# Optimization experiments

Hardware: AMD Instinct MI355X
Metric: run time of the kernel (lower is better)

The kernel has to match this reference:

```python
import jax, jax.numpy as jnp
import numpy as np

ORDER = 2  # diffusion steps per support
NUM_LAYERS = 2


def gconv(z, supports, W, b):
    # z: [B,N,C]; supports: [S,N,N]; concat [z, S1 z, S1^2 z, S2 z, S2^2 z] -> dense proj
    feats = [z]
    for si in range(supports.shape[0]):
        s = supports[si]
        zk = z
        for _ in range(ORDER):
            zk = jnp.einsum('mn,bnc->bmc', s, zk)
            feats.append(zk)
    zcat = jnp.concatenate(feats, axis=-1)  # [B,N,C*(1+S*ORDER)]
    return zcat @ W + b


def dcgru_cell(x, h, supports, Wg, bg, Wc, bc):
    H = h.shape[-1]
    zr = jax.nn.sigmoid(gconv(jnp.concatenate([x, h], axis=-1), supports, Wg, bg))
    z, r = zr[..., :H], zr[..., H:]
    hc = jnp.tanh(gconv(jnp.concatenate([x, r * h], axis=-1), supports, Wc, bc))
    return z * h + (1.0 - z) * hc


def setup_inputs() -> dict:
    key = jax.random.key(0)
    ks = jax.random.split(key, 32)
    B, T, N, D_IN, H = 64, 12, 325, 2, 128
    K = 1 + 2 * ORDER  # 5 diffusion matrices
    inp = {}
    inp['source'] = jax.random.normal(ks[0], (B, T, N, D_IN), jnp.float32)
    inp['targets'] = jax.random.normal(ks[1], (B, T, N, D_IN), jnp.float32)
    u = jax.random.uniform(ks[2], (2, N, N), jnp.float32)
    inp['supports'] = u / jnp.sum(u, axis=-1, keepdims=True)  # row-stochastic random walks
    sc = 0.05
    inp['enc_Wg0'] = sc * jax.random.normal(ks[3], ((D_IN + H) * K, 2 * H), jnp.float32)
    inp['enc_bg0'] = jnp.zeros((2 * H,), jnp.float32)
    inp['enc_Wc0'] = sc * jax.random.normal(ks[4], ((D_IN + H) * K, H), jnp.float32)
    inp['enc_bc0'] = jnp.zeros((H,), jnp.float32)
    inp['enc_Wg1'] = sc * jax.random.normal(ks[5], ((H + H) * K, 2 * H), jnp.float32)
    inp['enc_bg1'] = jnp.zeros((2 * H,), jnp.float32)
    inp['enc_Wc1'] = sc * jax.random.normal(ks[6], ((H + H) * K, H), jnp.float32)
    inp['enc_bc1'] = jnp.zeros((H,), jnp.float32)
    inp['dec_Wg0'] = sc * jax.random.normal(ks[7], ((D_IN + H) * K, 2 * H), jnp.float32)
    inp['dec_bg0'] = jnp.zeros((2 * H,), jnp.float32)
    inp['dec_Wc0'] = sc * jax.random.normal(ks[8], ((D_IN + H) * K, H), jnp.float32)
    inp['dec_bc0'] = jnp.zeros((H,), jnp.float32)
    inp['dec_Wg1'] = sc * jax.random.normal(ks[9], ((H + H) * K, 2 * H), jnp.float32)
    inp['dec_bg1'] = jnp.zeros((2 * H,), jnp.float32)
    inp['dec_Wc1'] = sc * jax.random.normal(ks[10], ((H + H) * K, H), jnp.float32)
    inp['dec_bc1'] = jnp.zeros((H,), jnp.float32)
    inp['Wp'] = sc * jax.random.normal(ks[11], (H, D_IN), jnp.float32)
    inp['bp'] = jnp.zeros((D_IN,), jnp.float32)
    return inp


def _forward(source, targets, supports,
             enc_Wg0, enc_bg0, enc_Wc0, enc_bc0, enc_Wg1, enc_bg1, enc_Wc1, enc_bc1,
             dec_Wg0, dec_bg0, dec_Wc0, dec_bc0, dec_Wg1, dec_bg1, dec_Wc1, dec_bc1,
             Wp, bp):
    B, T_in, N, D_in = source.shape
    T_out = targets.shape[1]
    enc_params = [(enc_Wg0, enc_bg0, enc_Wc0, enc_bc0), (enc_Wg1, enc_bg1, enc_Wc1, enc_bc1)]
    dec_params = [(dec_Wg0, dec_bg0, dec_Wc0, dec_bc0), (dec_Wg1, dec_bg1, dec_Wc1, dec_bc1)]

    # ---- encoder: per layer, scan over time ----
    cur = jnp.swapaxes(source, 0, 1)  # [T,B,N,C]
    enc_finals = []
    for (Wg, bg, Wc, bc) in enc_params:
        H = Wc.shape[-1]
        h0 = jnp.zeros((B, N, H), source.dtype)
        def step(h, xt, Wg=Wg, bg=bg, Wc=Wc, bc=bc):
            h2 = dcgru_cell(xt, h, supports, Wg, bg, Wc, bc)
            return h2, h2
        hT, hs = jax.lax.scan(step, h0, cur)
        enc_finals.append(hT)
        cur = hs

    # ---- decoder (teacher_forcing_ratio = 0 for determinism) ----
    out_dim = Wp.shape[-1]
    go = jnp.zeros((B, N, out_dim), source.dtype)  # GO symbol

    def dec_step(carry, _):
        states, cur_in = carry
        new_states = []
        x = cur_in
        for i, (Wg, bg, Wc, bc) in enumerate(dec_params):
            s = dcgru_cell(x, states[i], supports, Wg, bg, Wc, bc)
            x = s
            new_states.append(s)
        out = jnp.einsum('bnh,ho->bno', x, Wp) + bp  # [B,N,out_dim]
        return (tuple(new_states), out), out

    _, outs = jax.lax.scan(dec_step, (tuple(enc_finals), go), None, length=T_out)
    return jnp.swapaxes(outs, 0, 1)  # [B,T_out,N,out_dim]


def reference(source, targets, supports,
              enc_Wg0, enc_bg0, enc_Wc0, enc_bc0, enc_Wg1, enc_bg1, enc_Wc1, enc_bc1,
              dec_Wg0, dec_bg0, dec_Wc0, dec_bc0, dec_Wg1, dec_bg1, dec_Wc1, dec_bc1,
              Wp, bp):
    return _forward(source, targets, supports,
                    enc_Wg0, enc_bg0, enc_Wc0, enc_bc0, enc_Wg1, enc_bg1, enc_Wc1, enc_bc1,
                    dec_Wg0, dec_bg0, dec_Wc0, dec_bc0, dec_Wg1, dec_bg1, dec_Wc1, dec_bc1,
                    Wp, bp)
```

## Files before the change

kernel.cpp:

```cpp
#include <hip/hip_runtime.h>
#include <hip/hip_bf16.h>

#define B_  64
#define T_  12
#define N_  325
#define DIN 2
#define H_  128
#define BN  (B_*N_)
#define DPITCH 384
#define AROWS 384

typedef __hip_bfloat16 bf16;
typedef unsigned short u16;
typedef __attribute__((ext_vector_type(8))) short short8;
typedef __attribute__((ext_vector_type(4))) float f32x4;

__device__ __forceinline__ float b2f(bf16 v){ return __bfloat162float(v); }
__device__ __forceinline__ u16 f2b(float f){
    __hip_bfloat16 h = __float2bfloat16(f);
    return *reinterpret_cast<u16*>(&h);
}
__device__ __forceinline__ float ldf(const void* p, size_t i, int bf){
    return bf ? b2f(((const bf16*)p)[i]) : ((const float*)p)[i];
}

__device__ __forceinline__ void gl_lds16(const u16* g, u16* l){
    __builtin_amdgcn_global_load_lds(
        (const __attribute__((address_space(1))) unsigned int*)g,
        (__attribute__((address_space(3))) unsigned int*)l, 16, 0, 0);
}

struct FillCfg { u16 *F, *Ft; const float *x, *h; long xbs; int C, KC, Cpad, Din, b0, nb; };
struct DiffCfg { u16* F; const u16* Ft; int C, KC, Cpad, coff, ctiles, T, nb; };
struct GemmCfg { const u16* Fb; const u16* Wt; const float* bias; float* zr; float* hb;
                 int KC, KCpad, rows, gy, ct, nb; };
struct RhCfg  { u16 *F, *Ft; const float *zr, *h; int KC, Cpad, Din, b0, total, nb; };

__global__ void sniff(const void* __restrict__ sup, int* __restrict__ flag){
    if (threadIdx.x == 0 && blockIdx.x == 0){
        float sb = 0.f, sf = 0.f;
        for (int n = 0; n < N_; ++n){
            sb += b2f(((const bf16*)sup)[n]);
            sf += ((const float*)sup)[n];
        }
        float db = fabsf(sb - 1.f), df = fabsf(sf - 1.f);
        *flag = (db < df) ? 1 : 0;
    }
}

struct CvtArgs { const void* src[12]; float* dst[12]; int n[12]; };

__global__ void cvt_all(CvtArgs a, const int* __restrict__ flag){
    int ii = blockIdx.y;
    int i  = blockIdx.x*256 + threadIdx.x;
    if (i >= a.n[ii]) return;
    a.dst[ii][i] = ldf(a.src[ii], i, *flag);
}

__global__ void support_prep(const void* __restrict__ sup, const int* __restrict__ flag,
                             float* __restrict__ msq){
    int bf = *flag;
    int s = blockIdx.z;
    int m = blockIdx.y*16 + threadIdx.y;
    int n = blockIdx.x*16 + threadIdx.x;
    __shared__ float As[16][17], Bs[16][17];
    size_t base = (size_t)s*N_*N_;
    float acc = 0.f;
    for (int j0 = 0; j0 < N_; j0 += 16){
        As[threadIdx.y][threadIdx.x] = (m < N_ && j0+threadIdx.x < N_) ? ldf(sup, base + (size_t)m*N_ + j0+threadIdx.x, bf) : 0.f;
        Bs[threadIdx.y][threadIdx.x] = (j0+threadIdx.y < N_ && n < N_) ? ldf(sup, base + (size_t)(j0+threadIdx.y)*N_ + n, bf) : 0.f;
        __syncthreads();
        #pragma unroll
        for (int jj=0; jj<16; ++jj) acc += As[threadIdx.y][jj]*Bs[jj][threadIdx.x];
        __syncthreads();
    }
    if (m < N_ && n < N_){
        msq[(size_t)(2*s  )*N_*N_ + m*N_ + n] = ldf(sup, base + (size_t)m*N_ + n, bf);
        msq[(size_t)(2*s+1)*N_*N_ + m*N_ + n] = acc;
    }
}

__global__ void asq_prep(const float* __restrict__ msq, u16* __restrict__ asq){
    int idx = blockIdx.x*256 + threadIdx.x;
    int total = 4*AROWS*DPITCH;
    if (idx >= total) return;
    int col = idx % DPITCH;
    int rm  = idx / DPITCH;
    int m   = rm % AROWS;
    int k   = rm / AROWS;
    asq[idx] = (m < N_ && col < N_) ? f2b(msq[((size_t)k*N_ + m)*N_ + col]) : 0;
}

__global__ __launch_bounds__(256) void wtrans(const void* __restrict__ W, u16* __restrict__ Wt,
                                              int KC, int Nout, int KCpad,
                                              const int* __restrict__ flag){
    int bf = *flag;
    int k0 = blockIdx.x*64, c0 = blockIdx.y*64;
    int tid = threadIdx.x;
    __shared__ u16 T[64][72];
    #pragma unroll
    for (int it=0; it<2; ++it){
        int lin = it*256 + tid;
        int kl = lin >> 3, seg = lin & 7;
        int gk = k0 + kl, gc = c0 + seg*8;
        u16 tmp[8];
        #pragma unroll
        for (int e=0;e<8;++e) tmp[e] = (gk < KC) ? f2b(ldf(W, (size_t)gk*Nout + gc + e, bf)) : 0;
        *(uint4*)&T[kl][seg*8] = *(const uint4*)tmp;
    }
    __syncthreads();
    #pragma unroll
    for (int it=0; it<2; ++it){
        int lin = it*256 + tid;
        int cl = lin >> 3, seg = lin & 7;
        u16 tmp[8];
        #pragma unroll
        for (int j=0;j<8;++j) tmp[j] = T[seg*8+j][cl];
        *(uint4*)(Wt + (size_t)(c0+cl)*KCpad + k0 + seg*8) = *(const uint4*)tmp;
    }
}

__global__ __launch_bounds__(256) void fill_k(FillCfg ca, FillCfg cb, int na){
    int bi = blockIdx.x;
    FillCfg c = ca;
    if (bi >= na){ c = cb; bi -= na; }
    int gyc  = c.Cpad >> 6;
    int nblk = bi % 6;
    int rest = bi / 6;
    int cblk = rest % gyc;
    int bl   = rest / gyc;
    int bg = c.b0 + bl;
    int n0 = nblk*64, c0 = cblk*64;
    int tid = threadIdx.x;
    __shared__ u16 T[64][72];
    #pragma unroll
    for (int it=0; it<2; ++it){
        int lin = it*256 + tid;
        int nl = lin >> 3, seg = lin & 7;
        int gn = n0 + nl;
        u16 tmp[8];
        #pragma unroll
        for (int e=0;e<8;++e){
            int cc = c0 + seg*8 + e;
            float v = 0.f;
            if (gn < N_ && cc < c.C)
                v = (cc < c.Din) ? c.x[(size_t)bg*c.xbs + (size_t)gn*c.Din + cc]
                                 : c.h[((size_t)bg*N_ + gn)*H_ + (cc - c.Din)];
            tmp[e] = f2b(v);
        }
        *(uint4*)&T[nl][seg*8] = *(const uint4*)tmp;
        if (gn < N_){
            int cbase = c0 + seg*8;
            u16* dst = c.F + ((size_t)bl*N_ + gn)*c.KC + cbase;
            if (cbase + 7 < c.C){
                *(uint4*)dst = *(const uint4*)tmp;
            } else {
                #pragma unroll
                for (int e=0;e<8;++e) if (cbase + e < c.C) dst[e] = tmp[e];
            }
        }
    }
    __syncthreads();
    #pragma unroll
    for (int it=0; it<2; ++it){
        int lin = it*256 + tid;
        int cl = lin >> 3, seg = lin & 7;
        u16 tmp[8];
        #pragma unroll
        for (int j=0;j<8;++j) tmp[j] = T[seg*8+j][cl];
        *(uint4*)(c.Ft + (size_t)bl*c.Cpad*DPITCH + (size_t)(c0+cl)*DPITCH + n0 + seg*8)
            = *(const uint4*)tmp;
    }
}

__global__ void rh_k(RhCfg ca, RhCfg cb, int na){
    int blk = blockIdx.x;
    RhCfg c = ca;
    if (blk >= na){ c = cb; blk -= na; }
    int idx = blk*256 + threadIdx.x;
    if (idx >= c.total) return;
    int j   = idx & 127;
    int bnl = idx >> 7;
    int bl  = bnl / N_;
    int n   = bnl % N_;
    float r  = c.zr[(size_t)bnl*256 + 128 + j];
    float hv = c.h[((size_t)c.b0*N_ + bnl)*128 + j];
    u16 v = f2b(r * hv);
    c.F[(size_t)bnl*c.KC + c.Din + j] = v;
    c.Ft[((size_t)bl*c.Cpad + c.Din + j)*DPITCH + n] = v;
}

__global__ __launch_bounds__(256) void diffuse_k(DiffCfg ca, DiffCfg cb, int na,
                                                 const u16* __restrict__ asq){
    int bi = blockIdx.x;
    DiffCfg c = ca;
    if (bi >= na){ c = cb; bi -= na; }
    int xcd = bi & 7, m8 = bi >> 3;
    int tg = m8 / 12, s = m8 % 12;
    int t = tg*8 + xcd;
    if (t >= c.T) return;
    int bl = t / c.ctiles, cbk = t % c.ctiles;
    int y = s % 3, k = s / 3;

    const u16* A    = asq + (size_t)k*AROWS*DPITCH;
    const u16* Bt_g = c.Ft + ((size_t)bl*c.Cpad + c.coff)*DPITCH;
    u16*       Cm   = c.F + (size_t)bl*N_*c.KC + (size_t)(k+1)*c.C + c.coff;

    int m0 = y * 128;
    int c0 = cbk * 64;
    int tid = threadIdx.x;
    int wv = tid >> 6, lane = tid & 63, l15 = lane & 15, quad = lane >> 4;
    int lr = lane >> 3, ls = lane & 7;

    __shared__ u16 As[128*64];
    __shared__ u16 Bs[64*64];

    f32x4 acc[2][4];
    #pragma unroll
    for (int i2=0;i2<2;++i2)
        #pragma unroll
        for (int j=0;j<4;++j) acc[i2][j] = (f32x4){0.f,0.f,0.f,0.f};

    for (int k0 = 0; k0 < N_; k0 += 64){
        #pragma unroll
        for (int j=0;j<4;++j){
            int row = wv*32 + j*8 + lr;
            int seg = ls ^ lr;
            gl_lds16(A + (size_t)(m0+row)*DPITCH + k0 + seg*8, &As[(wv*32 + j*8)*64]);
        }
        #pragma unroll
        for (int j=0;j<2;++j){
            int row = wv*16 + j*8 + lr;
            int seg = ls ^ lr;
            gl_lds16(Bt_g + (size_t)(c0+row)*DPITCH + k0 + seg*8, &Bs[(wv*16 + j*8)*64]);
        }
        __syncthreads();
        #pragma unroll
        for (int ks = 0; ks < 64; ks += 32){
            int sw = (((ks>>3) + quad) ^ (l15 & 7)) << 3;
            short8 a0 = *(const short8*)&As[(wv*32      + l15)*64 + sw];
            short8 a1 = *(const short8*)&As[(wv*32 + 16 + l15)*64 + sw];
            short8 b0 = *(const short8*)&Bs[(     l15)*64 + sw];
            short8 b1 = *(const short8*)&Bs[(16 + l15)*64 + sw];
            short8 b2 = *(const short8*)&Bs[(32 + l15)*64 + sw];
            short8 b3 = *(const short8*)&Bs[(48 + l15)*64 + sw];
            acc[0][0] = __builtin_amdgcn_mfma_f32_16x16x32_bf16(a0,b0,acc[0][0],0,0,0);
            acc[0][1] = __builtin_amdgcn_mfma_f32_16x16x32_bf16(a0,b1,acc[0][1],0,0,0);
            acc[0][2] = __builtin_amdgcn_mfma_f32_16x16x32_bf16(a0,b2,acc[0][2],0,0,0);
            acc[0][3] = __builtin_amdgcn_mfma_f32_16x16x32_bf16(a0,b3,acc[0][3],0,0,0);
            acc[1][0] = __builtin_amdgcn_mfma_f32_16x16x32_bf16(a1,b0,acc[1][0],0,0,0);
            acc[1][1] = __builtin_amdgcn_mfma_f32_16x16x32_bf16(a1,b1,acc[1][1],0,0,0);
            acc[1][2] = __builtin_amdgcn_mfma_f32_16x16x32_bf16(a1,b2,acc[1][2],0,0,0);
            acc[1][3] = __builtin_amdgcn_mfma_f32_16x16x32_bf16(a1,b3,acc[1][3],0,0,0);
        }
        __syncthreads();
    }
    #pragma unroll
    for (int i2=0;i2<2;++i2){
        #pragma unroll
        for (int j=0;j<4;++j){
            int cc = c0 + j*16 + l15;
            #pragma unroll
            for (int r=0;r<4;++r){
                int m = m0 + wv*32 + i2*16 + quad*4 + r;
                if (m < N_ && c.coff + cc < c.C) Cm[(size_t)m*c.KC + cc] = f2b(acc[i2][j][r]);
            }
        }
    }
}

template<int MODE>
__global__ __launch_bounds__(256) void gemm_k(GemmCfg ca, GemmCfg cb, int na){
    int bi = blockIdx.x;
    GemmCfg c = ca;
    if (bi >= na){ c = cb; bi -= na; }
    int xcd = bi & 7, q = bi >> 3;
    int cbk = q % c.ct;
    int rt  = (q / c.ct)*8 + xcd;
    if (rt >= c.gy) return;
    int r0 = rt * 128;
    int c0 = cbk * 64;
    int tid = threadIdx.x;
    int wv = tid >> 6, lane = tid & 63, l15 = lane & 15, quad = lane >> 4;
    int lr = lane >> 3, ls = lane & 7;

    __shared__ u16 As[128*64];
    __shared__ u16 Bs[64*64];

    f32x4 acc[2][4];
    #pragma unroll
    for (int i2=0;i2<2;++i2)
        #pragma unroll
        for (int j=0;j<4;++j) acc[i2][j] = (f32x4){0.f,0.f,0.f,0.f};

    for (int k0 = 0; k0 < c.KCpad; k0 += 64){
        if (k0 + 64 <= c.KC){
            #pragma unroll
            for (int j=0;j<4;++j){
                int row = wv*32 + j*8 + lr;
                int seg = ls ^ lr;
                gl_lds16(c.Fb + (size_t)(r0+row)*c.KC + k0 + seg*8, &As[(wv*32 + j*8)*64]);
            }
        } else {
            #pragma unroll
            for (int it=0; it<4; ++it){
                int lin = it*256 + tid;
                int row = lin >> 3, sp = lin & 7;
                int seg = sp ^ (row & 7);
                int gr = r0 + row, gk = k0 + seg*8;
                u16 tmp[8];
                #pragma unroll
                for (int e=0;e<8;++e)
                    tmp[e] = (gk+e < c.KC) ? c.Fb[(size_t)gr*c.KC + gk+e] : (u16)0;
                *(uint4*)&As[row*64 + sp*8] = *(const uint4*)tmp;
            }
        }
        #pragma unroll
        for (int j=0;j<2;++j){
            int row = wv*16 + j*8 + lr;
            int seg = ls ^ lr;
            gl_lds16(c.Wt + (size_t)(c0+row)*c.KCpad + k0 + seg*8, &Bs[(wv*16 + j*8)*64]);
        }
        __syncthreads();
        #pragma unroll
        for (int ks = 0; ks < 64; ks += 32){
            int sw = (((ks>>3) + quad) ^ (l15 & 7)) << 3;
            short8 a0 = *(const short8*)&As[(wv*32      + l15)*64 + sw];
            short8 a1 = *(const short8*)&As[(wv*32 + 16 + l15)*64 + sw];
            short8 b0 = *(const short8*)&Bs[(     l15)*64 + sw];
            short8 b1 = *(const short8*)&Bs[(16 + l15)*64 + sw];
            short8 b2 = *(const short8*)&Bs[(32 + l15)*64 + sw];
            short8 b3 = *(const short8*)&Bs[(48 + l15)*64 + sw];
            acc[0][0] = __builtin_amdgcn_mfma_f32_16x16x32_bf16(a0,b0,acc[0][0],0,0,0);
            acc[0][1] = __builtin_amdgcn_mfma_f32_16x16x32_bf16(a0,b1,acc[0][1],0,0,0);
            acc[0][2] = __builtin_amdgcn_mfma_f32_16x16x32_bf16(a0,b2,acc[0][2],0,0,0);
            acc[0][3] = __builtin_amdgcn_mfma_f32_16x16x32_bf16(a0,b3,acc[0][3],0,0,0);
            acc[1][0] = __builtin_amdgcn_mfma_f32_16x16x32_bf16(a1,b0,acc[1][0],0,0,0);
            acc[1][1] = __builtin_amdgcn_mfma_f32_16x16x32_bf16(a1,b1,acc[1][1],0,0,0);
            acc[1][2] = __builtin_amdgcn_mfma_f32_16x16x32_bf16(a1,b2,acc[1][2],0,0,0);
            acc[1][3] = __builtin_amdgcn_mfma_f32_16x16x32_bf16(a1,b3,acc[1][3],0,0,0);
        }
        __syncthreads();
    }
    #pragma unroll
    for (int i2=0;i2<2;++i2){
        #pragma unroll
        for (int j=0;j<4;++j){
            int cc = c0 + j*16 + l15;
            #pragma unroll
            for (int r=0;r<4;++r){
                int gr = r0 + wv*32 + i2*16 + quad*4 + r;
                if (gr >= c.rows) continue;
                float v = acc[i2][j][r] + c.bias[cc];
                if (MODE == 0){
                    v = 1.f/(1.f + __expf(-v));
                    c.zr[(size_t)gr*256 + cc] = v;
                } else {
                    float hc   = tanhf(v);
                    float z    = c.zr[(size_t)gr*256 + cc];
                    float hold = c.hb[(size_t)gr*128 + cc];
                    c.hb[(size_t)gr*128 + cc] = z*hold + (1.f - z)*hc;
                }
            }
        }
    }
}

__global__ __launch_bounds__(256) void proj(const float* __restrict__ h1,
                                            const float* __restrict__ Wp,
                                            const float* __restrict__ bp,
                                            float* __restrict__ xdec,
                                            float* __restrict__ out, int t){
    int row  = blockIdx.x * 4 + (threadIdx.x >> 6);
    int lane = threadIdx.x & 63;
    float v0 = h1[(size_t)row*128 + lane];
    float v1 = h1[(size_t)row*128 + 64 + lane];
    float w00 = Wp[lane*2+0],      w01 = Wp[lane*2+1];
    float w10 = Wp[(64+lane)*2+0], w11 = Wp[(64+lane)*2+1];
    float a0 = v0*w00 + v1*w10;
    float a1 = v0*w01 + v1*w11;
    #pragma unroll
    for (int off=32; off>0; off>>=1){
        a0 += __shfl_down(a0, off);
        a1 += __shfl_down(a1, off);
    }
    if (lane == 0){
        a0 += bp[0];
        a1 += bp[1];
        xdec[(size_t)row*2+0] = a0;
        xdec[(size_t)row*2+1] = a1;
        int b = row / N_, n = row % N_;
        size_t o = ((size_t)(b*T_ + t)*N_ + n)*2;
        out[o]   = a0;
        out[o+1] = a1;
    }
}

struct Layer {
    u16 *F, *Ft; float *zr; float *h;
    const u16 *Wg, *Wc; const float *bg, *bc;
    int C, KC, KCpad, Din, ctiles, Cpad;
};

extern "C" void kernel_launch(void* const* d_in, const int* in_sizes, int n_in,
                              void* d_out, int out_size, void* d_ws, size_t ws_size,
                              hipStream_t stream){
    float* out = (float*)d_out;

    char* pb = (char*)d_ws;
    auto alloc = [&](size_t bytes)->void*{
        void* r = (void*)pb;
        pb += (bytes + 255) & ~(size_t)255;
        return r;
    };

    int* flag = (int*)alloc(16);
    sniff<<<1, 64, 0, stream>>>(d_in[2], flag);

    const int idxs[11] = {0,4,6,8,10,12,14,16,18,19,20};
    float* cw[21] = {nullptr};
    CvtArgs ca;
    int maxn = 0;
    for (int ii = 0; ii < 11; ++ii){
        int i = idxs[ii];
        int n = in_sizes[i];
        cw[i] = (float*)alloc((size_t)n*4);
        ca.src[ii] = d_in[i];
        ca.dst[ii] = cw[i];
        ca.n[ii]   = n;
        if (n > maxn) maxn = n;
    }
    cvt_all<<<dim3((maxn+255)/256, 11), 256, 0, stream>>>(ca, flag);
    const float* src = cw[0];

    float* msq  = (float*)alloc((size_t)4*N_*N_*4);
    float* h0   = (float*)alloc((size_t)BN*H_*4);
    float* h1   = (float*)alloc((size_t)BN*H_*4);
    float* xdec = (float*)alloc((size_t)BN*DIN*4);
    u16*   asq  = (u16*)alloc((size_t)4*AROWS*DPITCH*2);

    const int widx[8]  = {3,5,7,9,11,13,15,17};
    const int wKC[8]   = {650,650,1280,1280,650,650,1280,1280};
    const int wNout[8] = {256,128,256,128,256,128,256,128};
    u16* wt[8];
    for (int i=0;i<8;++i){
        int KCpad = (wKC[i] + 63) & ~63;
        wt[i] = (u16*)alloc((size_t)wNout[i]*KCpad*2);
        wtrans<<<dim3(KCpad/64, wNout[i]/64), 256, 0, stream>>>(d_in[widx[i]], wt[i], wKC[i], wNout[i], KCpad, flag);
    }

    {
        dim3 g((N_+15)/16, (N_+15)/16, 2), b(16,16);
        support_prep<<<g, b, 0, stream>>>(d_in[2], flag, msq);
        int tot = 4*AROWS*DPITCH;
        asq_prep<<<dim3((tot+255)/256), 256, 0, stream>>>(msq, asq);
    }
    hipMemsetAsync(h0, 0, sizeof(float)*(size_t)BN*H_*2, stream);

    size_t fixed = (size_t)(pb - (char*)d_ws);
    size_t need0 = (size_t)BN*256*4 + (size_t)BN*650*2  + (size_t)B_*192*DPITCH*2;
    size_t need1 = (size_t)BN*256*4 + (size_t)BN*1280*2 + (size_t)B_*256*DPITCH*2;
    bool dual = (fixed + need0 + need1 + (4<<20)) <= ws_size;

    auto mkFill = [&](Layer& L, const float* x, long xbs, int b0, int Bc)->FillCfg{
        return FillCfg{L.F, L.Ft, x, L.h, xbs, L.C, L.KC, L.Cpad, L.Din, b0,
                       6*(L.Cpad/64)*Bc};
    };
    auto mkD1 = [&](Layer& L, int Bc)->DiffCfg{
        int T = Bc*L.ctiles;
        return DiffCfg{L.F, L.Ft, L.C, L.KC, L.Cpad, 0, L.ctiles, T, 12*(((T+7)/8)*8)};
    };
    auto mkD2 = [&](Layer& L, int Bc)->DiffCfg{
        int T = Bc*2;
        return DiffCfg{L.F, L.Ft, L.C, L.KC, L.Cpad, L.Din, 2, T, 12*(((T+7)/8)*8)};
    };
    auto mkG0 = [&](Layer& L, int b0, int Bc)->GemmCfg{
        int rows = Bc*N_, gy = (rows+127)/128;
        return GemmCfg{L.F, L.Wg, L.bg, L.zr, L.h + (size_t)b0*N_*H_,
                       L.KC, L.KCpad, rows, gy, 4, 8*((gy+7)/8)*4};
    };
    auto mkG1 = [&](Layer& L, int b0, int Bc)->GemmCfg{
        int rows = Bc*N_, gy = (rows+127)/128;
        return GemmCfg{L.F, L.Wc, L.bc, L.zr, L.h + (size_t)b0*N_*H_,
                       L.KC, L.KCpad, rows, gy, 2, 8*((gy+7)/8)*2};
    };
    auto mkRh = [&](Layer& L, int b0, int Bc)->RhCfg{
        int total = Bc*N_*H_;
        return RhCfg{L.F, L.Ft, L.zr, L.h, L.KC, L.Cpad, L.Din, b0, total, (total+255)/256};
    };
    auto runCellSeq = [&](Layer& L, const float* x, long xbs, int b0, int Bc){
        FillCfg f = mkFill(L, x, xbs, b0, Bc);
        fill_k<<<dim3(f.nb), 256, 0, stream>>>(f, f, f.nb);
        DiffCfg d1 = mkD1(L, Bc);
        diffuse_k<<<dim3(d1.nb), 256, 0, stream>>>(d1, d1, d1.nb, asq);
        GemmCfg g0 = mkG0(L, b0, Bc);
        gemm_k<0><<<dim3(g0.nb), 256, 0, stream>>>(g0, g0, g0.nb);
        RhCfg r = mkRh(L, b0, Bc);
        rh_k<<<dim3(r.nb), 256, 0, stream>>>(r, r, r.nb);
        DiffCfg d2 = mkD2(L, Bc);
        diffuse_k<<<dim3(d2.nb), 256, 0, stream>>>(d2, d2, d2.nb, asq);
        GemmCfg g1 = mkG1(L, b0, Bc);
        gemm_k<1><<<dim3(g1.nb), 256, 0, stream>>>(g1, g1, g1.nb);
    };

    if (dual){
        float* zr0 = (float*)alloc((size_t)BN*256*4);
        u16*   F0  = (u16*)alloc((size_t)BN*650*2);
        u16*   Ft0 = (u16*)alloc((size_t)B_*192*DPITCH*2);
        float* zr1 = (float*)alloc((size_t)BN*256*4);
        u16*   F1  = (u16*)alloc((size_t)BN*1280*2);
        u16*   Ft1 = (u16*)alloc((size_t)B_*256*DPITCH*2);
        alloc(1<<19);

        Layer E0{F0, Ft0, zr0, h0, wt[0], wt[1], cw[4],  cw[6],  130, 650, 704, 2,   3, 192};
        Layer E1{F1, Ft1, zr1, h1, wt[2], wt[3], cw[8],  cw[10], 256, 1280,1280,128, 4, 256};
        Layer D0{F0, Ft0, zr0, h0, wt[4], wt[5], cw[12], cw[14], 130, 650, 704, 2,   3, 192};
        Layer D1{F1, Ft1, zr1, h1, wt[6], wt[7], cw[16], cw[18], 256, 1280,1280,128, 4, 256};

        for (int s = 0; s <= T_; ++s){
            bool has0 = (s < T_), has1 = (s >= 1);
            const float* x0 = src + (size_t)s*N_*DIN;
            FillCfg f0 = mkFill(E0, x0, (long)T_*N_*DIN, 0, B_);
            FillCfg f1 = mkFill(E1, h0, (long)N_*H_,     0, B_);
            if (has0 && has1) fill_k<<<dim3(f0.nb+f1.nb),256,0,stream>>>(f0, f1, f0.nb);
            else if (has0)    fill_k<<<dim3(f0.nb),256,0,stream>>>(f0, f0, f0.nb);
            else              fill_k<<<dim3(f1.nb),256,0,stream>>>(f1, f1, f1.nb);

            DiffCfg a1 = mkD1(E0, B_), b1 = mkD1(E1, B_);
            if (has0 && has1) diffuse_k<<<dim3(a1.nb+b1.nb),256,0,stream>>>(a1, b1, a1.nb, asq);
            else if (has0)    diffuse_k<<<dim3(a1.nb),256,0,stream>>>(a1, a1, a1.nb, asq);
            else              diffuse_k<<<dim3(b1.nb),256,0,stream>>>(b1, b1, b1.nb, asq);

            GemmCfg ga = mkG0(E0, 0, B_), gb = mkG0(E1, 0, B_);
            if (has0 && has1) gemm_k<0><<<dim3(ga.nb+gb.nb),256,0,stream>>>(ga, gb, ga.nb);
            else if (has0)    gemm_k<0><<<dim3(ga.nb),256,0,stream>>>(ga, ga, ga.nb);
            else              gemm_k<0><<<dim3(gb.nb),256,0,stream>>>(gb, gb, gb.nb);

            RhCfg ra = mkRh(E0, 0, B_), rb = mkRh(E1, 0, B_);
            if (has0 && has1) rh_k<<<dim3(ra.nb+rb.nb),256,0,stream>>>(ra, rb, ra.nb);
            else if (has0)    rh_k<<<dim3(ra.nb),256,0,stream>>>(ra, ra, ra.nb);
            else              rh_k<<<dim3(rb.nb),256,0,stream>>>(rb, rb, rb.nb);

            DiffCfg a2 = mkD2(E0, B_), b2 = mkD2(E1, B_);
            if (has0 && has1) diffuse_k<<<dim3(a2.nb+b2.nb),256,0,stream>>>(a2, b2, a2.nb, asq);
            else if (has0)    diffuse_k<<<dim3(a2.nb),256,0,stream>>>(a2, a2, a2.nb, asq);
            else              diffuse_k<<<dim3(b2.nb),256,0,stream>>>(b2, b2, b2.nb, asq);

            GemmCfg ha = mkG1(E0, 0, B_), hb = mkG1(E1, 0, B_);
            if (has0 && has1) gemm_k<1><<<dim3(ha.nb+hb.nb),256,0,stream>>>(ha, hb, ha.nb);
            else if (has0)    gemm_k<1><<<dim3(ha.nb),256,0,stream>>>(ha, ha, ha.nb);
            else              gemm_k<1><<<dim3(hb.nb),256,0,stream>>>(hb, hb, hb.nb);
        }

        hipMemsetAsync(xdec, 0, sizeof(float)*(size_t)BN*DIN, stream);
        for (int t = 0; t < T_; ++t){
            runCellSeq(D0, xdec, (long)N_*DIN, 0, B_);
            runCellSeq(D1, h0,   (long)N_*H_,  0, B_);
            proj<<<dim3(BN/4), 256, 0, stream>>>(h1, cw[19], cw[20], xdec, out, t);
        }
    } else {
        size_t perb = (size_t)N_*1280*2 + (size_t)N_*256*4 + (size_t)256*DPITCH*2;
        int Bc = 64;
        while (Bc > 2 && fixed + (1<<20) + (size_t)Bc*perb > ws_size) Bc >>= 1;
        float* zr = (float*)alloc((size_t)Bc*N_*256*4);
        u16*   F  = (u16*)alloc((size_t)Bc*N_*1280*2);
        u16*   Ft = (u16*)alloc((size_t)Bc*256*DPITCH*2);
        alloc(1<<19);

        Layer SE0{F, Ft, zr, h0, wt[0], wt[1], cw[4],  cw[6],  130, 650, 704, 2,   3, 192};
        Layer SE1{F, Ft, zr, h1, wt[2], wt[3], cw[8],  cw[10], 256, 1280,1280,128, 4, 256};
        Layer SD0{F, Ft, zr, h0, wt[4], wt[5], cw[12], cw[14], 130, 650, 704, 2,   3, 192};
        Layer SD1{F, Ft, zr, h1, wt[6], wt[7], cw[16], cw[18], 256, 1280,1280,128, 4, 256};

        for (int t = 0; t < T_; ++t){
            for (int b0 = 0; b0 < B_; b0 += Bc)
                runCellSeq(SE0, src + (size_t)t*N_*DIN, (long)T_*N_*DIN, b0, Bc);
            for (int b0 = 0; b0 < B_; b0 += Bc)
                runCellSeq(SE1, h0, (long)N_*H_, b0, Bc);
        }
        hipMemsetAsync(xdec, 0, sizeof(float)*(size_t)BN*DIN, stream);
        for (int t = 0; t < T_; ++t){
            for (int b0 = 0; b0 < B_; b0 += Bc)
                runCellSeq(SD0, xdec, (long)N_*DIN, b0, Bc);
            for (int b0 = 0; b0 < B_; b0 += Bc)
                runCellSeq(SD1, h0, (long)N_*H_, b0, Bc);
            proj<<<dim3(BN/4), 256, 0, stream>>>(h1, cw[19], cw[20], xdec, out, t);
        }
    }
}
```

Before: 5.919 ms.

## Reorder channel layout so decoder h-diffusion overlaps with layer-1 and x-diffusion is tiny

Permutes the feature concatenation order (h first, x last) via weight-row permutation in wtrans, so the hidden-state part of layer-0 decoder features can be filled and diffused early, batched together with the layer-1 fill/diffuse of the previous step. A new small diffx_k kernel diffuses only the 2-channel projected output each step, and proj writes xdec directly into the feature buffer. This removes the separate full layer-0 fill and reduces serialized launches in the decoder loop, at the cost of added layout complexity and a dedicated low-utilization MFMA kernel for 2 channels.

```diff
diff --git a/kernel.cpp b/kernel.cpp
--- a/kernel.cpp
+++ b/kernel.cpp
@@ -30,11 +30,12 @@
         (__attribute__((address_space(3))) unsigned int*)l, 16, 0, 0);
 }
 
-struct FillCfg { u16 *F, *Ft; const float *x, *h; long xbs; int C, KC, Cpad, Din, b0, nb; };
+struct FillCfg { u16 *F, *Ft; const float *x, *h; long xbs;
+                 int C, KC, Cpad, xoff, xdim, hoff, ftiles, b0, nb; };
 struct DiffCfg { u16* F; const u16* Ft; int C, KC, Cpad, coff, ctiles, T, nb; };
 struct GemmCfg { const u16* Fb; const u16* Wt; const float* bias; float* zr; float* hb;
                  int KC, KCpad, rows, gy, ct, nb; };
-struct RhCfg  { u16 *F, *Ft; const float *zr, *h; int KC, Cpad, Din, b0, total, nb; };
+struct RhCfg  { u16 *F, *Ft; const float *zr, *h; int KC, Cpad, hoff, b0, total, nb; };
 
 __global__ void sniff(const void* __restrict__ sup, int* __restrict__ flag){
     if (threadIdx.x == 0 && blockIdx.x == 0){
@@ -92,7 +93,7 @@
 }
 
 __global__ __launch_bounds__(256) void wtrans(const void* __restrict__ W, u16* __restrict__ Wt,
-                                              int KC, int Nout, int KCpad,
+                                              int KC, int Nout, int KCpad, int permC,
                                               const int* __restrict__ flag){
     int bf = *flag;
     int k0 = blockIdx.x*64, c0 = blockIdx.y*64;
@@ -104,8 +105,19 @@
         int kl = lin >> 3, seg = lin & 7;
         int gk = k0 + kl, gc = c0 + seg*8;
         u16 tmp[8];
-        #pragma unroll
-        for (int e=0;e<8;++e) tmp[e] = (gk < KC) ? f2b(ldf(W, (size_t)gk*Nout + gc + e, bf)) : 0;
+        int ok = (gk < KC);
+        size_t orow = 0;
+        if (ok){
+            int r = gk;
+            if (permC > 0){
+                int s  = gk / permC;
+                int lo = gk % permC;
+                r = s*permC + ((lo < 128) ? lo + 2 : lo - 128);
+            }
+            orow = (size_t)r * Nout;
+        }
+        #pragma unroll
+        for (int e=0;e<8;++e) tmp[e] = ok ? f2b(ldf(W, orow + gc + e, bf)) : 0;
         *(uint4*)&T[kl][seg*8] = *(const uint4*)tmp;
     }
     __syncthreads();
@@ -124,11 +136,10 @@
     int bi = blockIdx.x;
     FillCfg c = ca;
     if (bi >= na){ c = cb; bi -= na; }
-    int gyc  = c.Cpad >> 6;
     int nblk = bi % 6;
     int rest = bi / 6;
-    int cblk = rest % gyc;
-    int bl   = rest / gyc;
+    int cblk = rest % c.ftiles;
+    int bl   = rest / c.ftiles;
     int bg = c.b0 + bl;
     int n0 = nblk*64, c0 = cblk*64;
     int tid = threadIdx.x;
@@ -143,9 +154,12 @@
         for (int e=0;e<8;++e){
             int cc = c0 + seg*8 + e;
             float v = 0.f;
-            if (gn < N_ && cc < c.C)
-                v = (cc < c.Din) ? c.x[(size_t)bg*c.xbs + (size_t)gn*c.Din + cc]
-                                 : c.h[((size_t)bg*N_ + gn)*H_ + (cc - c.Din)];
+            if (gn < N_){
+                if (cc >= c.xoff && cc < c.xoff + c.xdim)
+                    v = c.x[(size_t)bg*c.xbs + (size_t)gn*c.xdim + (cc - c.xoff)];
+                else if (cc >= c.hoff && cc < c.hoff + 128)
+                    v = c.h[((size_t)bg*N_ + gn)*H_ + (cc - c.hoff)];
+            }
             tmp[e] = f2b(v);
         }
         *(uint4*)&T[nl][seg*8] = *(const uint4*)tmp;
@@ -186,8 +200,8 @@
     float r  = c.zr[(size_t)bnl*256 + 128 + j];
     float hv = c.h[((size_t)c.b0*N_ + bnl)*128 + j];
     u16 v = f2b(r * hv);
-    c.F[(size_t)bnl*c.KC + c.Din + j] = v;
-    c.Ft[((size_t)bl*c.Cpad + c.Din + j)*DPITCH + n] = v;
+    c.F[(size_t)bnl*c.KC + c.hoff + j] = v;
+    c.Ft[((size_t)bl*c.Cpad + c.hoff + j)*DPITCH + n] = v;
 }
 
 __global__ __launch_bounds__(256) void diffuse_k(DiffCfg ca, DiffCfg cb, int na,
@@ -269,6 +283,75 @@
     }
 }
 
+__global__ __launch_bounds__(256) void diffx_k(u16* __restrict__ F,
+                                               const float* __restrict__ xdec,
+                                               const u16* __restrict__ asq,
+                                               int C, int KC, int coff){
+    int bi = blockIdx.x;
+    int xcd = bi & 7, m8 = bi >> 3;
+    int tg = m8 / 12, s = m8 % 12;
+    int t = tg*8 + xcd;
+    if (t >= B_) return;
+    int bl = t;
+    int y = s % 3, k = s / 3;
+
+    const u16* A  = asq + (size_t)k*AROWS*DPITCH;
+    u16*       Cm = F + (size_t)bl*N_*KC + (size_t)(k+1)*C + coff;
+
+    int m0 = y * 128;
+    int tid = threadIdx.x;
+    int wv = tid >> 6, lane = tid & 63, l15 = lane & 15, quad = lane >> 4;
+    int lr = lane >> 3, ls = lane & 7;
+
+    __shared__ u16 As[128*64];
+    __shared__ u16 Bs[64*64];
+
+    f32x4 acc0 = (f32x4){0.f,0.f,0.f,0.f};
+    f32x4 acc1 = (f32x4){0.f,0.f,0.f,0.f};
+
+    for (int k0 = 0; k0 < N_; k0 += 64){
+        #pragma unroll
+        for (int j=0;j<4;++j){
+            int row = wv*32 + j*8 + lr;
+            int seg = ls ^ lr;
+            gl_lds16(A + (size_t)(m0+row)*DPITCH + k0 + seg*8, &As[(wv*32 + j*8)*64]);
+        }
+        #pragma unroll
+        for (int i=0;i<16;++i){
+            int lin = tid*16 + i;
+            int row = lin >> 6;
+            int kk  = lin & 63;
+            u16 v = 0;
+            if (row < 2 && k0 + kk < N_)
+                v = f2b(xdec[((size_t)bl*N_ + k0 + kk)*2 + row]);
+            int seg = kk >> 3, e = kk & 7;
+            Bs[row*64 + ((seg ^ (row&7))<<3) + e] = v;
+        }
+        __syncthreads();
+        #pragma unroll
+        for (int ks = 0; ks < 64; ks += 32){
+            int sw = (((ks>>3) + quad) ^ (l15 & 7)) << 3;
+            short8 a0 = *(const short8*)&As[(wv*32      + l15)*64 + sw];
+            short8 a1 = *(const short8*)&As[(wv*32 + 16 + l15)*64 + sw];
+            short8 b0 = *(const short8*)&Bs[(     l15)*64 + sw];
+            acc0 = __builtin_amdgcn_mfma_f32_16x16x32_bf16(a0,b0,acc0,0,0,0);
+            acc1 = __builtin_amdgcn_mfma_f32_16x16x32_bf16(a1,b0,acc1,0,0,0);
+        }
+        __syncthreads();
+    }
+    if (l15 < 2){
+        #pragma unroll
+        for (int i2=0;i2<2;++i2){
+            f32x4 a = i2 ? acc1 : acc0;
+            #pragma unroll
+            for (int r=0;r<4;++r){
+                int m = m0 + wv*32 + i2*16 + quad*4 + r;
+                if (m < N_) Cm[(size_t)m*KC + l15] = f2b(a[r]);
+            }
+        }
+    }
+}
+
 template<int MODE>
 __global__ __launch_bounds__(256) void gemm_k(GemmCfg ca, GemmCfg cb, int na){
     int bi = blockIdx.x;
@@ -370,7 +453,8 @@
                                             const float* __restrict__ Wp,
                                             const float* __restrict__ bp,
                                             float* __restrict__ xdec,
-                                            float* __restrict__ out, int t){
+                                            float* __restrict__ out, int t,
+                                            u16* __restrict__ F0x, int KC0, int xoff){
     int row  = blockIdx.x * 4 + (threadIdx.x >> 6);
     int lane = threadIdx.x & 63;
     float v0 = h1[(size_t)row*128 + lane];
@@ -389,6 +473,10 @@
         a1 += bp[1];
         xdec[(size_t)row*2+0] = a0;
         xdec[(size_t)row*2+1] = a1;
+        if (F0x){
+            F0x[(size_t)row*KC0 + xoff    ] = f2b(a0);
+            F0x[(size_t)row*KC0 + xoff + 1] = f2b(a1);
+        }
         int b = row / N_, n = row % N_;
         size_t o = ((size_t)(b*T_ + t)*N_ + n)*2;
         out[o]   = a0;
@@ -396,10 +484,17 @@
     }
 }
 
+__global__ void go_init(float* __restrict__ xdec, u16* __restrict__ F0, int KC0, int xoff){
+    int i = blockIdx.x*256 + threadIdx.x;
+    if (i >= BN) return;
+    xdec[2*i] = 0.f; xdec[2*i+1] = 0.f;
+    F0[(size_t)i*KC0 + xoff] = 0; F0[(size_t)i*KC0 + xoff + 1] = 0;
+}
+
 struct Layer {
     u16 *F, *Ft; float *zr; float *h;
     const u16 *Wg, *Wc; const float *bg, *bc;
-    int C, KC, KCpad, Din, ctiles, Cpad;
+    int C, KC, KCpad, ctiles, Cpad, xoff, xdim, hoff;
 };
 
 extern "C" void kernel_launch(void* const* d_in, const int* in_sizes, int n_in,
@@ -442,11 +537,12 @@
     const int widx[8]  = {3,5,7,9,11,13,15,17};
     const int wKC[8]   = {650,650,1280,1280,650,650,1280,1280};
     const int wNout[8] = {256,128,256,128,256,128,256,128};
+    const int wPerm[8] = {130,130,0,0,130,130,0,0};
     u16* wt[8];
     for (int i=0;i<8;++i){
         int KCpad = (wKC[i] + 63) & ~63;
         wt[i] = (u16*)alloc((size_t)wNout[i]*KCpad*2);
-        wtrans<<<dim3(KCpad/64, wNout[i]/64), 256, 0, stream>>>(d_in[widx[i]], wt[i], wKC[i], wNout[i], KCpad, flag);
+        wtrans<<<dim3(KCpad/64, wNout[i]/64), 256, 0, stream>>>(d_in[widx[i]], wt[i], wKC[i], wNout[i], KCpad, wPerm[i], flag);
     }
 
     {
@@ -462,42 +558,39 @@
     size_t need1 = (size_t)BN*256*4 + (size_t)BN*1280*2 + (size_t)B_*256*DPITCH*2;
     bool dual = (fixed + need0 + need1 + (4<<20)) <= ws_size;
 
-    auto mkFill = [&](Layer& L, const float* x, long xbs, int b0, int Bc)->FillCfg{
-        return FillCfg{L.F, L.Ft, x, L.h, xbs, L.C, L.KC, L.Cpad, L.Din, b0,
-                       6*(L.Cpad/64)*Bc};
+    auto ceil8 = [](int x){ return ((x+7)/8)*8; };
+    auto mkFill = [&](Layer& L, const float* x, long xbs, int b0, int Bc, int ftiles)->FillCfg{
+        return FillCfg{L.F, L.Ft, x, L.h, xbs, L.C, L.KC, L.Cpad,
+                       L.xoff, L.xdim, L.hoff, ftiles, b0, 6*ftiles*Bc};
     };
-    auto mkD1 = [&](Layer& L, int Bc)->DiffCfg{
-        int T = Bc*L.ctiles;
-        return DiffCfg{L.F, L.Ft, L.C, L.KC, L.Cpad, 0, L.ctiles, T, 12*(((T+7)/8)*8)};
-    };
-    auto mkD2 = [&](Layer& L, int Bc)->DiffCfg{
-        int T = Bc*2;
-        return DiffCfg{L.F, L.Ft, L.C, L.KC, L.Cpad, L.Din, 2, T, 12*(((T+7)/8)*8)};
+    auto mkDiff = [&](Layer& L, int Bc, int coff, int ct)->DiffCfg{
+        int T = Bc*ct;
+        return DiffCfg{L.F, L.Ft, L.C, L.KC, L.Cpad, coff, ct, T, 12*ceil8(T)};
     };
     auto mkG0 = [&](Layer& L, int b0, int Bc)->GemmCfg{
         int rows = Bc*N_, gy = (rows+127)/128;
         return GemmCfg{L.F, L.Wg, L.bg, L.zr, L.h + (size_t)b0*N_*H_,
-                       L.KC, L.KCpad, rows, gy, 4, 8*((gy+7)/8)*4};
+                       L.KC, L.KCpad, rows, gy, 4, ceil8(gy)*4};
     };
     auto mkG1 = [&](Layer& L, int b0, int Bc)->GemmCfg{
         int rows = Bc*N_, gy = (rows+127)/128;
         return GemmCfg{L.F, L.Wc, L.bc, L.zr, L.h + (size_t)b0*N_*H_,
-                       L.KC, L.KCpad, rows, gy, 2, 8*((gy+7)/8)*2};
+                       L.KC, L.KCpad, rows, gy, 2, ceil8(gy)*2};
     };
     auto mkRh = [&](Layer& L, int b0, int Bc)->RhCfg{
         int total = Bc*N_*H_;
-        return RhCfg{L.F, L.Ft, L.zr, L.h, L.KC, L.Cpad, L.Din, b0, total, (total+255)/256};
+        return RhCfg{L.F, L.Ft, L.zr, L.h, L.KC, L.Cpad, L.hoff, b0, total, (total+255)/256};
     };
     auto runCellSeq = [&](Layer& L, const float* x, long xbs, int b0, int Bc){
-        FillCfg f = mkFill(L, x, xbs, b0, Bc);
+        FillCfg f = mkFill(L, x, xbs, b0, Bc, L.Cpad/64);
         fill_k<<<dim3(f.nb), 256, 0, stream>>>(f, f, f.nb);
-        DiffCfg d1 = mkD1(L, Bc);
+        DiffCfg d1 = mkDiff(L, Bc, 0, L.ctiles);
         diffuse_k<<<dim3(d1.nb), 256, 0, stream>>>(d1, d1, d1.nb, asq);
         GemmCfg g0 = mkG0(L, b0, Bc);
         gemm_k<0><<<dim3(g0.nb), 256, 0, stream>>>(g0, g0, g0.nb);
         RhCfg r = mkRh(L, b0, Bc);
         rh_k<<<dim3(r.nb), 256, 0, stream>>>(r, r, r.nb);
-        DiffCfg d2 = mkD2(L, Bc);
+        DiffCfg d2 = mkDiff(L, Bc, L.hoff, 2);
         diffuse_k<<<dim3(d2.nb), 256, 0, stream>>>(d2, d2, d2.nb, asq);
         GemmCfg g1 = mkG1(L, b0, Bc);
         gemm_k<1><<<dim3(g1.nb), 256, 0, stream>>>(g1, g1, g1.nb);
@@ -512,21 +605,21 @@
         u16*   Ft1 = (u16*)alloc((size_t)B_*256*DPITCH*2);
         alloc(1<<19);
 
-        Layer E0{F0, Ft0, zr0, h0, wt[0], wt[1], cw[4],  cw[6],  130, 650, 704, 2,   3, 192};
-        Layer E1{F1, Ft1, zr1, h1, wt[2], wt[3], cw[8],  cw[10], 256, 1280,1280,128, 4, 256};
-        Layer D0{F0, Ft0, zr0, h0, wt[4], wt[5], cw[12], cw[14], 130, 650, 704, 2,   3, 192};
-        Layer D1{F1, Ft1, zr1, h1, wt[6], wt[7], cw[16], cw[18], 256, 1280,1280,128, 4, 256};
+        Layer E0{F0, Ft0, zr0, h0, wt[0], wt[1], cw[4],  cw[6],  130, 650, 704, 3, 192, 128, 2,   0};
+        Layer E1{F1, Ft1, zr1, h1, wt[2], wt[3], cw[8],  cw[10], 256, 1280,1280, 4, 256, 0,   128, 128};
+        Layer D0{F0, Ft0, zr0, h0, wt[4], wt[5], cw[12], cw[14], 130, 650, 704, 3, 192, 128, 2,   0};
+        Layer D1{F1, Ft1, zr1, h1, wt[6], wt[7], cw[16], cw[18], 256, 1280,1280, 4, 256, 0,   128, 128};
 
         for (int s = 0; s <= T_; ++s){
             bool has0 = (s < T_), has1 = (s >= 1);
             const float* x0 = src + (size_t)s*N_*DIN;
-            FillCfg f0 = mkFill(E0, x0, (long)T_*N_*DIN, 0, B_);
-            FillCfg f1 = mkFill(E1, h0, (long)N_*H_,     0, B_);
+            FillCfg f0 = mkFill(E0, x0, (long)T_*N_*DIN, 0, B_, 3);
+            FillCfg f1 = mkFill(E1, h0, (long)N_*H_,     0, B_, 4);
             if (has0 && has1) fill_k<<<dim3(f0.nb+f1.nb),256,0,stream>>>(f0, f1, f0.nb);
             else if (has0)    fill_k<<<dim3(f0.nb),256,0,stream>>>(f0, f0, f0.nb);
             else              fill_k<<<dim3(f1.nb),256,0,stream>>>(f1, f1, f1.nb);
 
-            DiffCfg a1 = mkD1(E0, B_), b1 = mkD1(E1, B_);
+            DiffCfg a1 = mkDiff(E0, B_, 0, 3), b1 = mkDiff(E1, B_, 0, 4);
             if (has0 && has1) diffuse_k<<<dim3(a1.nb+b1.nb),256,0,stream>>>(a1, b1, a1.nb, asq);
             else if (has0)    diffuse_k<<<dim3(a1.nb),256,0,stream>>>(a1, a1, a1.nb, asq);
             else              diffuse_k<<<dim3(b1.nb),256,0,stream>>>(b1, b1, b1.nb, asq);
@@ -541,7 +634,7 @@
             else if (has0)    rh_k<<<dim3(ra.nb),256,0,stream>>>(ra, ra, ra.nb);
             else              rh_k<<<dim3(rb.nb),256,0,stream>>>(rb, rb, rb.nb);
 
-            DiffCfg a2 = mkD2(E0, B_), b2 = mkD2(E1, B_);
+            DiffCfg a2 = mkDiff(E0, B_, 0, 2), b2 = mkDiff(E1, B_, 128, 2);
             if (has0 && has1) diffuse_k<<<dim3(a2.nb+b2.nb),256,0,stream>>>(a2, b2, a2.nb, asq);
             else if (has0)    diffuse_k<<<dim3(a2.nb),256,0,stream>>>(a2, a2, a2.nb, asq);
             else              diffuse_k<<<dim3(b2.nb),256,0,stream>>>(b2, b2, b2.nb, asq);
@@ -552,11 +645,46 @@
             else              gemm_k<1><<<dim3(hb.nb),256,0,stream>>>(hb, hb, hb.nb);
         }
 
-        hipMemsetAsync(xdec, 0, sizeof(float)*(size_t)BN*DIN, stream);
+        go_init<<<dim3((BN+255)/256), 256, 0, stream>>>(xdec, F0, 650, 128);
+        {
+            FillCfg fh = mkFill(D0, xdec, (long)N_*DIN, 0, B_, 2);
+            fill_k<<<dim3(fh.nb), 256, 0, stream>>>(fh, fh, fh.nb);
+            DiffCfg dh = mkDiff(D0, B_, 0, 2);
+            diffuse_k<<<dim3(dh.nb), 256, 0, stream>>>(dh, dh, dh.nb, asq);
+        }
         for (int t = 0; t < T_; ++t){
-            runCellSeq(D0, xdec, (long)N_*DIN, 0, B_);
-            runCellSeq(D1, h0,   (long)N_*H_,  0, B_);
-            proj<<<dim3(BN/4), 256, 0, stream>>>(h1, cw[19], cw[20], xdec, out, t);
+            int nbx = 12*64;
+            diffx_k<<<dim3(nbx), 256, 0, stream>>>(F0, xdec, asq, 130, 650, 128);
+            GemmCfg g0a = mkG0(D0, 0, B_);
+            gemm_k<0><<<dim3(g0a.nb),256,0,stream>>>(g0a, g0a, g0a.nb);
+            RhCfg r0c = mkRh(D0, 0, B_);
+            rh_k<<<dim3(r0c.nb),256,0,stream>>>(r0c, r0c, r0c.nb);
+            DiffCfg d2a = mkDiff(D0, B_, 0, 2);
+            diffuse_k<<<dim3(d2a.nb),256,0,stream>>>(d2a, d2a, d2a.nb, asq);
+            GemmCfg g1a = mkG1(D0, 0, B_);
+            gemm_k<1><<<dim3(g1a.nb),256,0,stream>>>(g1a, g1a, g1a.nb);
+
+            FillCfg f1c = mkFill(D1, h0, (long)N_*H_, 0, B_, 4);
+            DiffCfg d1c = mkDiff(D1, B_, 0, 4);
+            if (t < T_-1){
+                FillCfg fh = mkFill(D0, xdec, (long)N_*DIN, 0, B_, 2);
+                fill_k<<<dim3(f1c.nb+fh.nb),256,0,stream>>>(f1c, fh, f1c.nb);
+                DiffCfg dh = mkDiff(D0, B_, 0, 2);
+                diffuse_k<<<dim3(d1c.nb+dh.nb),256,0,stream>>>(d1c, dh, d1c.nb, asq);
+            } else {
+                fill_k<<<dim3(f1c.nb),256,0,stream>>>(f1c, f1c, f1c.nb);
+                diffuse_k<<<dim3(d1c.nb),256,0,stream>>>(d1c, d1c, d1c.nb, asq);
+            }
+            GemmCfg g0b = mkG0(D1, 0, B_);
+            gemm_k<0><<<dim3(g0b.nb),256,0,stream>>>(g0b, g0b, g0b.nb);
+            RhCfg r1c = mkRh(D1, 0, B_);
+            rh_k<<<dim3(r1c.nb),256,0,stream>>>(r1c, r1c, r1c.nb);
+            DiffCfg d2b = mkDiff(D1, B_, 128, 2);
+            diffuse_k<<<dim3(d2b.nb),256,0,stream>>>(d2b, d2b, d2b.nb, asq);
+            GemmCfg g1b = mkG1(D1, 0, B_);
+            gemm_k<1><<<dim3(g1b.nb),256,0,stream>>>(g1b, g1b, g1b.nb);
+
+            proj<<<dim3(BN/4), 256, 0, stream>>>(h1, cw[19], cw[20], xdec, out, t, F0, 650, 128);
         }
     } else {
         size_t perb = (size_t)N_*1280*2 + (size_t)N_*256*4 + (size_t)256*DPITCH*2;
@@ -567,10 +695,10 @@
         u16*   Ft = (u16*)alloc((size_t)Bc*256*DPITCH*2);
         alloc(1<<19);
 
-        Layer SE0{F, Ft, zr, h0, wt[0], wt[1], cw[4],  cw[6],  130, 650, 704, 2,   3, 192};
-        Layer SE1{F, Ft, zr, h1, wt[2], wt[3], cw[8],  cw[10], 256, 1280,1280,128, 4, 256};
-        Layer SD0{F, Ft, zr, h0, wt[4], wt[5], cw[12], cw[14], 130, 650, 704, 2,   3, 192};
-        Layer SD1{F, Ft, zr, h1, wt[6], wt[7], cw[16], cw[18], 256, 1280,1280,128, 4, 256};
+        Layer SE0{F, Ft, zr, h0, wt[0], wt[1], cw[4],  cw[6],  130, 650, 704, 3, 192, 128, 2,   0};
+        Layer SE1{F, Ft, zr, h1, wt[2], wt[3], cw[8],  cw[10], 256, 1280,1280, 4, 256, 0,   128, 128};
+        Layer SD0{F, Ft, zr, h0, wt[4], wt[5], cw[12], cw[14], 130, 650, 704, 3, 192, 128, 2,   0};
+        Layer SD1{F, Ft, zr, h1, wt[6], wt[7], cw[16], cw[18], 256, 1280,1280, 4, 256, 0,   128, 128};
 
         for (int t = 0; t < T_; ++t){
             for (int b0 = 0; b0 < B_; b0 += Bc)
@@ -584,7 +712,8 @@
                 runCellSeq(SD0, xdec, (long)N_*DIN, b0, Bc);
             for (int b0 = 0; b0 < B_; b0 += Bc)
                 runCellSeq(SD1, h0, (long)N_*H_, b0, Bc);
-            proj<<<dim3(BN/4), 256, 0, stream>>>(h1, cw[19], cw[20], xdec, out, t);
-        }
-    }
-}
+            proj<<<dim3(BN/4), 256, 0, stream>>>(h1, cw[19], cw[20], xdec, out, t,
+                                                 (u16*)nullptr, 650, 128);
+        }
+    }
+}
```

After: 5.953 ms. About the same (+0.6%).
